# Kernel tuning notes

Hardware: AMD Instinct MI355X
Metric: run time of the kernel (lower is better)

The kernel has to match this reference:

```python
import jax, jax.numpy as jnp
import numpy as np

KERNEL_SIZE = 5


def _box_sum(x, k):
    """Sum over a k x k window with zero padding k//2 (== conv2d with all-ones kernel)."""
    pad = k // 2
    return jax.lax.reduce_window(
        x, 0.0, jax.lax.add,
        window_dimensions=(1, 1, k, k),
        window_strides=(1, 1, 1, 1),
        padding=[(0, 0), (0, 0), (pad, pad), (pad, pad)],
    )


def setup_inputs() -> dict:
    key = jax.random.key(0)
    k1, k2 = jax.random.split(key)
    B, C, H, W = 32, 1, 512, 512
    pred = jax.random.normal(k1, (B, C, H, W), dtype=jnp.float32)
    # binary {0,1} target mask, as required by binary_cross_entropy
    target = (jax.random.uniform(k2, (B, C, H, W)) > 0.5).astype(jnp.float32)
    return {"pred": pred, "target": target}


def reference(pred, target):
    k = KERNEL_SIZE
    # Morphological boundary: original code runs the same all-ones conv twice;
    # compute the box-sum once (identical math).
    s = _box_sum(target, k)                      # [B,1,H,W]
    dilated = (s > 0).astype(pred.dtype)
    eroded = (s == float(k * k)).astype(pred.dtype)
    boundary = dilated - eroded

    p = jax.nn.sigmoid(pred)
    # torch F.binary_cross_entropy clamps each log term at -100
    log_p = jnp.clip(jnp.log(p), -100.0, None)
    log_1mp = jnp.clip(jnp.log1p(-p), -100.0, None)
    bce = -(target * log_p + (1.0 - target) * log_1mp)

    boundary_weight = boundary * 4.0 + 1.0
    return jnp.mean(bce * boundary_weight)
```

## Files before the change

kernel.cpp:

```cpp
#include <hip/hip_runtime.h>
#include <math.h>


typedef unsigned long long u64;
typedef float v4f __attribute__((ext_vector_type(4)));

constexpr int NB = 32, H = 512, W = 512;
constexpr int RPW = 4;
constexpr int SPI = H / RPW;
constexpr int WPB = 4;
constexpr int NBLK = NB * SPI / WPB;
constexpr float INV_N = 1.0f / (float)(NB * H * W);

__device__ __forceinline__ u64 pack8(v4f a, v4f b) {
    unsigned a0 = __builtin_bit_cast(unsigned, a.x), a1 = __builtin_bit_cast(unsigned, a.y),
             a2 = __builtin_bit_cast(unsigned, a.z), a3 = __builtin_bit_cast(unsigned, a.w);
    unsigned b0 = __builtin_bit_cast(unsigned, b.x), b1 = __builtin_bit_cast(unsigned, b.y),
             b2 = __builtin_bit_cast(unsigned, b.z), b3 = __builtin_bit_cast(unsigned, b.w);
    unsigned lo = ((a0 >> 23) & 0x1u)      | ((a1 >> 15) & 0x100u)
                | ((a2 >> 7)  & 0x10000u)  | ((a3 << 1)  & 0x1000000u);
    unsigned hi = ((b0 >> 23) & 0x1u)      | ((b1 >> 15) & 0x100u)
                | ((b2 >> 7)  & 0x10000u)  | ((b3 << 1)  & 0x1000000u);
    return (u64)lo | ((u64)hi << 32);
}

__device__ __forceinline__ float bce_one(float x, unsigned tbit, unsigned s) {
    float y = tbit ? -x : x;
    float sp = fmaxf(y, 0.0f) + __logf(1.0f + __expf(-fabsf(y)));
    float w = (s - 1u) < 24u ? 5.0f : 1.0f;
    return w * fminf(sp, 100.0f);
}

__global__ __launch_bounds__(256, 4) void bl_main(
    const float* __restrict__ pred, const float* __restrict__ tgt,
    float* __restrict__ partials)
{
    const int tid  = threadIdx.x;
    const int lane = tid & 63;
    const int widx = tid >> 6;
    const int blk  = blockIdx.x;
    const int gs   = (blk & 7) * (NBLK / 8 * WPB) + (blk >> 3) * WPB + widx;
    const int b    = gs >> 7;
    const int r0   = (gs & (SPI - 1)) * RPW;
    const int c    = lane * 8;
    const float* tb = tgt  + (size_t)b * H * W;
    const float* pb = pred + (size_t)b * H * W;

    u64 hring[5], vring[5];
    float acc = 0.0f;

#pragma unroll
    for (int i = 0; i < RPW + 4; ++i) {
        const int r = r0 - 2 + i;
        u64 v = 0;
        if ((unsigned)r < (unsigned)H) {
            const v4f* tp = (const v4f*)(tb + (size_t)r * W + c);
            v = pack8(tp[0], tp[1]);
        }
        u64 lv = __shfl_up(v, 1, 64);
        u64 rv = __shfl_down(v, 1, 64);
        if (lane == 0)  lv = 0;
        if (lane == 63) rv = 0;
        u64 h = v + ((v << 8) | (lv >> 56)) + ((v << 16) | (lv >> 48))
                  + ((v >> 8) | (rv << 56)) + ((v >> 16) | (rv << 48));
        hring[i % 5] = h;
        vring[i % 5] = v;

        if (i >= 4) {
            const int ro = r0 + i - 4;
            u64 S  = hring[0] + hring[1] + hring[2] + hring[3] + hring[4];
            u64 vc = vring[(i + 3) % 5];
            const v4f* pp = (const v4f*)(pb + (size_t)ro * W + c);
            v4f p0 = __builtin_nontemporal_load(pp);
            v4f p1 = __builtin_nontemporal_load(pp + 1);
            unsigned vl = (unsigned)vc,         Sl = (unsigned)S;
            unsigned vh = (unsigned)(vc >> 32), Sh = (unsigned)(S >> 32);
            acc += bce_one(p0.x,  vl        & 1u,  Sl        & 0xFFu);
            acc += bce_one(p0.y, (vl >>  8) & 1u, (Sl >>  8) & 0xFFu);
            acc += bce_one(p0.z, (vl >> 16) & 1u, (Sl >> 16) & 0xFFu);
            acc += bce_one(p0.w, (vl >> 24) & 1u, (Sl >> 24) & 0xFFu);
            acc += bce_one(p1.x,  vh        & 1u,  Sh        & 0xFFu);
            acc += bce_one(p1.y, (vh >>  8) & 1u, (Sh >>  8) & 0xFFu);
            acc += bce_one(p1.z, (vh >> 16) & 1u, (Sh >> 16) & 0xFFu);
            acc += bce_one(p1.w, (vh >> 24) & 1u, (Sh >> 24) & 0xFFu);
        }
    }

    #pragma unroll
    for (int off = 32; off > 0; off >>= 1)
        acc += __shfl_down(acc, off, 64);
    __shared__ float wsum[WPB];
    if (lane == 0) wsum[widx] = acc;
    __syncthreads();
    if (tid == 0)
        partials[blk] = wsum[0] + wsum[1] + wsum[2] + wsum[3];
}

__global__ __launch_bounds__(256) void bl_final(
    const float* __restrict__ p, float* __restrict__ out)
{
    const int tid = threadIdx.x;
    float v = p[tid] + p[tid + 256] + p[tid + 512] + p[tid + 768];
    #pragma unroll
    for (int off = 32; off > 0; off >>= 1)
        v += __shfl_down(v, off, 64);
    __shared__ float wsum[4];
    if ((tid & 63) == 0) wsum[tid >> 6] = v;
    __syncthreads();
    if (tid == 0)
        out[0] = (wsum[0] + wsum[1] + wsum[2] + wsum[3]) * INV_N;
}

extern "C" void kernel_launch(void* const* d_in, const int* in_sizes, int n_in,
                              void* d_out, int out_size, void* d_ws, size_t ws_size,
                              hipStream_t stream) {
    const float* pred = (const float*)d_in[0];
    const float* tgt  = (const float*)d_in[1];
    float* partials = (float*)d_ws;
    float* out = (float*)d_out;

    bl_main<<<NBLK, 256, 0, stream>>>(pred, tgt, partials);
    bl_final<<<1, 256, 0, stream>>>(partials, out);
}
```

Before: 102.3 us.

## Fuse final reduction into main kernel via flags and double rows per wave

Result: no change. 103.8 us (+1.5%).

```diff
diff --git a/kernel.cpp b/kernel.cpp
--- a/kernel.cpp
+++ b/kernel.cpp
@@ -6,7 +6,7 @@
 typedef float v4f __attribute__((ext_vector_type(4)));
 
 constexpr int NB = 32, H = 512, W = 512;
-constexpr int RPW = 4;
+constexpr int RPW = 8;
 constexpr int SPI = H / RPW;
 constexpr int WPB = 4;
 constexpr int NBLK = NB * SPI / WPB;
@@ -31,17 +31,18 @@
     return w * fminf(sp, 100.0f);
 }
 
-__global__ __launch_bounds__(256, 4) void bl_main(
+__global__ __launch_bounds__(256, 2) void bl_main(
     const float* __restrict__ pred, const float* __restrict__ tgt,
-    float* __restrict__ partials)
+    float* __restrict__ partials, unsigned* __restrict__ flags,
+    float* __restrict__ out)
 {
     const int tid  = threadIdx.x;
     const int lane = tid & 63;
     const int widx = tid >> 6;
     const int blk  = blockIdx.x;
-    const int gs   = (blk & 7) * (NBLK / 8 * WPB) + (blk >> 3) * WPB + widx;
-    const int b    = gs >> 7;
-    const int r0   = (gs & (SPI - 1)) * RPW;
+    const int g    = blk * WPB + widx;
+    const int b    = g >> 6;
+    const int r0   = (g & (SPI - 1)) * RPW;
     const int c    = lane * 8;
     const float* tb = tgt  + (size_t)b * H * W;
     const float* pb = pred + (size_t)b * H * W;
@@ -71,8 +72,7 @@
             u64 S  = hring[0] + hring[1] + hring[2] + hring[3] + hring[4];
             u64 vc = vring[(i + 3) % 5];
             const v4f* pp = (const v4f*)(pb + (size_t)ro * W + c);
-            v4f p0 = __builtin_nontemporal_load(pp);
-            v4f p1 = __builtin_nontemporal_load(pp + 1);
+            v4f p0 = pp[0], p1 = pp[1];
             unsigned vl = (unsigned)vc,         Sl = (unsigned)S;
             unsigned vh = (unsigned)(vc >> 32), Sh = (unsigned)(S >> 32);
             acc += bce_one(p0.x,  vl        & 1u,  Sl        & 0xFFu);
@@ -92,23 +92,26 @@
     __shared__ float wsum[WPB];
     if (lane == 0) wsum[widx] = acc;
     __syncthreads();
-    if (tid == 0)
+    if (tid == 0) {
         partials[blk] = wsum[0] + wsum[1] + wsum[2] + wsum[3];
-}
+        __hip_atomic_store(&flags[blk], 1u, __ATOMIC_RELEASE, __HIP_MEMORY_SCOPE_AGENT);
+    }
 
-__global__ __launch_bounds__(256) void bl_final(
-    const float* __restrict__ p, float* __restrict__ out)
-{
-    const int tid = threadIdx.x;
-    float v = p[tid] + p[tid + 256] + p[tid + 512] + p[tid + 768];
-    #pragma unroll
-    for (int off = 32; off > 0; off >>= 1)
-        v += __shfl_down(v, off, 64);
-    __shared__ float wsum[4];
-    if ((tid & 63) == 0) wsum[tid >> 6] = v;
-    __syncthreads();
-    if (tid == 0)
-        out[0] = (wsum[0] + wsum[1] + wsum[2] + wsum[3]) * INV_N;
+    if (blk == NBLK - 1) {
+        #pragma unroll
+        for (int i = tid; i < NBLK; i += 256)
+            while (__hip_atomic_load(&flags[i], __ATOMIC_ACQUIRE,
+                                     __HIP_MEMORY_SCOPE_AGENT) != 1u) {}
+        __syncthreads();
+        float v = partials[tid] + partials[tid + 256];
+        #pragma unroll
+        for (int off = 32; off > 0; off >>= 1)
+            v += __shfl_down(v, off, 64);
+        if (lane == 0) wsum[widx] = v;
+        __syncthreads();
+        if (tid == 0)
+            out[0] = (wsum[0] + wsum[1] + wsum[2] + wsum[3]) * INV_N;
+    }
 }
 
 extern "C" void kernel_launch(void* const* d_in, const int* in_sizes, int n_in,
@@ -116,9 +119,9 @@
                               hipStream_t stream) {
     const float* pred = (const float*)d_in[0];
     const float* tgt  = (const float*)d_in[1];
-    float* partials = (float*)d_ws;
+    float* partials  = (float*)d_ws;
+    unsigned* flags  = (unsigned*)d_ws + 512;
     float* out = (float*)d_out;
 
-    bl_main<<<NBLK, 256, 0, stream>>>(pred, tgt, partials);
-    bl_final<<<1, 256, 0, stream>>>(partials, out);
+    bl_main<<<NBLK, 256, 0, stream>>>(pred, tgt, partials, flags, out);
 }
```
